# Kernel optimization log

Measured on AMD Instinct MI355X. Metric: run time of the kernel, lower is better.

The kernel has to match this reference:

```python
import jax, jax.numpy as jnp
import numpy as np

N_NODES = 50000


def sage_conv(x, src, dst, W_l, b_l, W_r, n_nodes):
    """PyG SAGEConv with mean aggregation: lin_l(mean_{j->i} x_j) + lin_r(x_i)."""
    msg = x[src]                                            # [E, d]
    agg = jax.ops.segment_sum(msg, dst, num_segments=n_nodes)
    cnt = jax.ops.segment_sum(jnp.ones((src.shape[0],), x.dtype), dst,
                              num_segments=n_nodes)
    agg = agg / jnp.maximum(cnt, 1.0)[:, None]              # mean over in-neighbors
    return agg @ W_l.T + b_l + x @ W_r.T


def setup_inputs() -> dict:
    key = jax.random.key(0)
    ks = jax.random.split(key, 8)
    d_in, d_hid, d_out = 128, 128, 64
    E = 600000
    x = jax.random.normal(ks[0], (N_NODES, d_in), dtype=jnp.float32)
    edge_index = jax.random.randint(ks[1], (2, E), 0, N_NODES, dtype=jnp.int64)
    s = 1.0 / np.sqrt(d_in)
    return {
        "x": x,
        "edge_index": edge_index,
        "W1_l": jax.random.normal(ks[2], (d_hid, d_in), jnp.float32) * s,
        "b1": jnp.zeros((d_hid,), jnp.float32),
        "W1_r": jax.random.normal(ks[3], (d_hid, d_in), jnp.float32) * s,
        "W2_l": jax.random.normal(ks[4], (d_out, d_hid), jnp.float32) * s,
        "b2": jnp.zeros((d_out,), jnp.float32),
        "W2_r": jax.random.normal(ks[5], (d_out, d_hid), jnp.float32) * s,
    }


def reference(x, edge_index, W1_l, b1, W1_r, W2_l, b2, W2_r):
    src, dst = edge_index[0], edge_index[1]
    h = sage_conv(x, src, dst, W1_l, b1, W1_r, N_NODES)
    h = jax.nn.relu(h)
    h = sage_conv(h, src, dst, W2_l, b2, W2_r, N_NODES)
    return jax.nn.log_softmax(h, axis=1)
```

## Files before the change

kernel.cpp:

```cpp
#include <hip/hip_runtime.h>
#include <math.h>

#define N_NODES 50000
#define D 128
#define D_OUT 64

typedef short bf16x8 __attribute__((ext_vector_type(8)));
typedef float f32x4  __attribute__((ext_vector_type(4)));
typedef unsigned short u16x8 __attribute__((ext_vector_type(8)));

__device__ __forceinline__ unsigned short f_to_bf16(float f) {
    unsigned int u = __float_as_uint(f);
    u = (u + 0x7fffu + ((u >> 16) & 1u)) >> 16;
    return (unsigned short)u;
}
__device__ __forceinline__ float bf16lo(unsigned int v) { return __uint_as_float(v << 16); }
__device__ __forceinline__ float bf16hi(unsigned int v) { return __uint_as_float(v & 0xffff0000u); }

__device__ __forceinline__ void conv8(const float* __restrict__ src, unsigned short* __restrict__ dst, int i)
{
    float4 v0 = *reinterpret_cast<const float4*>(src + i);
    float4 v1 = *reinterpret_cast<const float4*>(src + i + 4);
    u16x8 o;
    o[0] = f_to_bf16(v0.x); o[1] = f_to_bf16(v0.y);
    o[2] = f_to_bf16(v0.z); o[3] = f_to_bf16(v0.w);
    o[4] = f_to_bf16(v1.x); o[5] = f_to_bf16(v1.y);
    o[6] = f_to_bf16(v1.z); o[7] = f_to_bf16(v1.w);
    *reinterpret_cast<u16x8*>(dst + i) = o;
}

__device__ __forceinline__ void acc_add(float* acc, uint4 v)
{
    acc[0] += bf16lo(v.x); acc[1] += bf16hi(v.x);
    acc[2] += bf16lo(v.y); acc[3] += bf16hi(v.y);
    acc[4] += bf16lo(v.z); acc[5] += bf16hi(v.z);
    acc[6] += bf16lo(v.w); acc[7] += bf16hi(v.w);
}

__global__ __launch_bounds__(256) void zero_kernel(int* __restrict__ p, int n4)
{
    int i = blockIdx.x * 256 + threadIdx.x;
    if (i < n4) *reinterpret_cast<int4*>(p + i * 4) = make_int4(0, 0, 0, 0);
}

__global__ __launch_bounds__(256) void prep_kernel(
    const float* __restrict__ x, unsigned short* __restrict__ xb,
    const float* __restrict__ w1l, const float* __restrict__ w1r,
    const float* __restrict__ w2l, const float* __restrict__ w2r,
    unsigned short* __restrict__ Wb,
    const int* __restrict__ dst, int* __restrict__ deg,
    int XB, int E)
{
    const int bx = blockIdx.x;
    if (bx < XB) {
        int i = (bx * 256 + threadIdx.x) * 8;
        if (i < N_NODES * D) conv8(x, xb, i);
    } else if (bx < XB + 24) {
        int i = ((bx - XB) * 256 + threadIdx.x) * 8;
        const float* src; int off;
        if      (i < 16384) { src = w1l; off = 0; }
        else if (i < 32768) { src = w1r; off = 16384; }
        else if (i < 40960) { src = w2l; off = 32768; }
        else                { src = w2r; off = 40960; }
        conv8(src, Wb + off, i - off);
    } else {
        int e = (bx - XB - 24) * 256 + threadIdx.x;
        if (e < E) atomicAdd(&deg[dst[e]], 1);
    }
}

__global__ __launch_bounds__(256) void scan1_kernel(
    const int* __restrict__ deg, int* __restrict__ part,
    int* __restrict__ bsum, int n)
{
    const int t = threadIdx.x;
    const int base = blockIdx.x * 1024 + t * 4;

    int a0 = 0, a1 = 0, a2 = 0, a3 = 0;
    if (base + 3 < n) {
        int4 v = *reinterpret_cast<const int4*>(deg + base);
        a0 = v.x; a1 = v.y; a2 = v.z; a3 = v.w;
    } else if (base < n) {
        a0 = deg[base];
        if (base + 1 < n) a1 = deg[base + 1];
        if (base + 2 < n) a2 = deg[base + 2];
    }
    const int s0 = a0, s1 = s0 + a1, s2 = s1 + a2, s3 = s2 + a3;

    const int lane = t & 63;
    int incl = s3;
#pragma unroll
    for (int off = 1; off < 64; off <<= 1) {
        int up = __shfl_up(incl, off);
        if (lane >= off) incl += up;
    }

    __shared__ int wsum[4];
    const int wid = t >> 6;
    if (lane == 63) wsum[wid] = incl;
    __syncthreads();

    int woff = 0;
#pragma unroll
    for (int w = 0; w < 4; ++w) woff += (w < wid) ? wsum[w] : 0;

    const int ex = woff + incl - s3;
    if (base + 3 < n) {
        int4 o; o.x = ex; o.y = ex + s0; o.z = ex + s1; o.w = ex + s2;
        *reinterpret_cast<int4*>(part + base) = o;
    } else if (base < n) {
        part[base] = ex;
        if (base + 1 < n) part[base + 1] = ex + s0;
        if (base + 2 < n) part[base + 2] = ex + s1;
    }
    if (t == 255) bsum[blockIdx.x] = woff + incl;
}

__global__ __launch_bounds__(64) void scan2_kernel(
    int* __restrict__ bsum, int* __restrict__ row_ptr, int nb, int n)
{
    const int t = threadIdx.x;
    int v = (t < nb) ? bsum[t] : 0;
    int incl = v;
#pragma unroll
    for (int off = 1; off < 64; off <<= 1) {
        int up = __shfl_up(incl, off);
        if (t >= off) incl += up;
    }
    if (t < nb) bsum[t] = incl - v;
    if (t == 63) row_ptr[n] = incl;
}

__global__ __launch_bounds__(256) void scan3_kernel(
    const int* __restrict__ part, const int* __restrict__ bsum,
    int* __restrict__ row_ptr, int n)
{
    const int base = blockIdx.x * 1024 + threadIdx.x * 4;
    const int add = bsum[blockIdx.x];
    if (base + 3 < n) {
        int4 v = *reinterpret_cast<const int4*>(part + base);
        v.x += add; v.y += add; v.z += add; v.w += add;
        *reinterpret_cast<int4*>(row_ptr + base) = v;
    } else if (base < n) {
        row_ptr[base] = part[base] + add;
        if (base + 1 < n) row_ptr[base + 1] = part[base + 1] + add;
        if (base + 2 < n) row_ptr[base + 2] = part[base + 2] + add;
    }
}

__global__ __launch_bounds__(256) void fill_kernel(
    const int* __restrict__ src, const int* __restrict__ dst,
    const int* __restrict__ row_ptr, int* __restrict__ cursor,
    int* __restrict__ esrc, int E)
{
    int e = blockIdx.x * blockDim.x + threadIdx.x;
    if (e >= E) return;
    int d = dst[e];
    int pos = atomicAdd(&cursor[d], 1);
    esrc[row_ptr[d] + pos] = src[e];
}

__global__ __launch_bounds__(256) void gather_bf16_kernel(
    const unsigned short* __restrict__ xb,
    const int* __restrict__ row_ptr,
    const int* __restrict__ esrc,
    unsigned short* __restrict__ aggb,
    int n_nodes)
{
    const int wv   = threadIdx.x >> 6;
    const int lane = threadIdx.x & 63;
    const int node = blockIdx.x * 4 + wv;
    if (node >= n_nodes) return;

    const int beg = row_ptr[node];
    const int end = row_ptr[node + 1];
    const int g = lane >> 4;
    const int c = lane & 15;

    const uint4* x4 = reinterpret_cast<const uint4*>(xb);

    float acc[8];
#pragma unroll
    for (int k = 0; k < 8; ++k) acc[k] = 0.f;

    for (int base = beg; base < end; base += 64) {
        const int cnt = min(end - base, 64);
        int s = (base + lane < end) ? esrc[base + lane] : 0;
        for (int i = 0; i < cnt; i += 8) {
            const int p0 = i + g;
            const int p1 = i + 4 + g;
            const int s0 = __shfl(s, p0 & 63);
            const int s1 = __shfl(s, p1 & 63);
            uint4 v0 = x4[(size_t)s0 * 16 + c];
            uint4 v1 = x4[(size_t)s1 * 16 + c];
            if (p0 < cnt) acc_add(acc, v0);
            if (p1 < cnt) acc_add(acc, v1);
        }
    }

#pragma unroll
    for (int k = 0; k < 8; ++k) {
        acc[k] += __shfl_xor(acc[k], 16);
        acc[k] += __shfl_xor(acc[k], 32);
    }

    if (g == 0) {
        const float inv = (end > beg) ? 1.0f / (float)(end - beg) : 0.0f;
        uint4 o;
        o.x = (unsigned int)f_to_bf16(acc[0] * inv) | ((unsigned int)f_to_bf16(acc[1] * inv) << 16);
        o.y = (unsigned int)f_to_bf16(acc[2] * inv) | ((unsigned int)f_to_bf16(acc[3] * inv) << 16);
        o.z = (unsigned int)f_to_bf16(acc[4] * inv) | ((unsigned int)f_to_bf16(acc[5] * inv) << 16);
        o.w = (unsigned int)f_to_bf16(acc[6] * inv) | ((unsigned int)f_to_bf16(acc[7] * inv) << 16);
        reinterpret_cast<uint4*>(aggb)[(size_t)node * 16 + c] = o;
    }
}

__global__ __launch_bounds__(64) void layer1_mfma_kernel(
    const unsigned short* __restrict__ aggb,
    const unsigned short* __restrict__ xb,
    const unsigned short* __restrict__ Wb,
    const float* __restrict__ b1,
    unsigned short* __restrict__ h1b)
{
    const int lane  = threadIdx.x;
    const int node0 = blockIdx.x * 16;
    const int c16   = lane & 15;
    const int kg    = lane >> 4;

    bf16x8 a[2][4];
    {
        const unsigned short* A0 = aggb + (size_t)(node0 + c16) * D + kg * 8;
        const unsigned short* A1 = xb   + (size_t)(node0 + c16) * D + kg * 8;
#pragma unroll
        for (int kf = 0; kf < 4; ++kf) {
            a[0][kf] = *reinterpret_cast<const bf16x8*>(A0 + kf * 32);
            a[1][kf] = *reinterpret_cast<const bf16x8*>(A1 + kf * 32);
        }
    }
    const unsigned short* WL = Wb;
    const unsigned short* WR = Wb + 16384;

#pragma unroll 2
    for (int jt = 0; jt < 8; ++jt) {
        f32x4 acc = {0.f, 0.f, 0.f, 0.f};
        const unsigned short* wl = WL + (size_t)(jt * 16 + c16) * D + kg * 8;
        const unsigned short* wr = WR + (size_t)(jt * 16 + c16) * D + kg * 8;
#pragma unroll
        for (int kf = 0; kf < 4; ++kf) {
            bf16x8 b = *reinterpret_cast<const bf16x8*>(wl + kf * 32);
            acc = __builtin_amdgcn_mfma_f32_16x16x32_bf16(a[0][kf], b, acc, 0, 0, 0);
        }
#pragma unroll
        for (int kf = 0; kf < 4; ++kf) {
            bf16x8 b = *reinterpret_cast<const bf16x8*>(wr + kf * 32);
            acc = __builtin_amdgcn_mfma_f32_16x16x32_bf16(a[1][kf], b, acc, 0, 0, 0);
        }
        const float bias = b1[jt * 16 + c16];
#pragma unroll
        for (int i = 0; i < 4; ++i) {
            float v = fmaxf(acc[i] + bias, 0.0f);
            h1b[(size_t)(node0 + kg * 4 + i) * D + jt * 16 + c16] = f_to_bf16(v);
        }
    }
}

__global__ __launch_bounds__(64) void layer2_mfma_kernel(
    const unsigned short* __restrict__ aggb,
    const unsigned short* __restrict__ h1b,
    const unsigned short* __restrict__ Wb,
    const float* __restrict__ b2,
    float* __restrict__ out)
{
    const int lane  = threadIdx.x;
    const int node0 = blockIdx.x * 16;
    const int c16   = lane & 15;
    const int kg    = lane >> 4;

    bf16x8 a[2][4];
    {
        const unsigned short* A0 = aggb + (size_t)(node0 + c16) * D + kg * 8;
        const unsigned short* A1 = h1b  + (size_t)(node0 + c16) * D + kg * 8;
#pragma unroll
        for (int kf = 0; kf < 4; ++kf) {
            a[0][kf] = *reinterpret_cast<const bf16x8*>(A0 + kf * 32);
            a[1][kf] = *reinterpret_cast<const bf16x8*>(A1 + kf * 32);
        }
    }
    const unsigned short* WL = Wb + 32768;
    const unsigned short* WR = Wb + 40960;

    f32x4 accs[4];
#pragma unroll
    for (int jt = 0; jt < 4; ++jt) {
        f32x4 acc = {0.f, 0.f, 0.f, 0.f};
        const unsigned short* wl = WL + (size_t)(jt * 16 + c16) * D + kg * 8;
        const unsigned short* wr = WR + (size_t)(jt * 16 + c16) * D + kg * 8;
#pragma unroll
        for (int kf = 0; kf < 4; ++kf) {
            bf16x8 b = *reinterpret_cast<const bf16x8*>(wl + kf * 32);
            acc = __builtin_amdgcn_mfma_f32_16x16x32_bf16(a[0][kf], b, acc, 0, 0, 0);
        }
#pragma unroll
        for (int kf = 0; kf < 4; ++kf) {
            bf16x8 b = *reinterpret_cast<const bf16x8*>(wr + kf * 32);
            acc = __builtin_amdgcn_mfma_f32_16x16x32_bf16(a[1][kf], b, acc, 0, 0, 0);
        }
        accs[jt] = acc;
    }

    float bias[4];
#pragma unroll
    for (int jt = 0; jt < 4; ++jt) bias[jt] = b2[jt * 16 + c16];

#pragma unroll
    for (int i = 0; i < 4; ++i) {
        float z[4];
        float m = -1e30f;
#pragma unroll
        for (int jt = 0; jt < 4; ++jt) {
            z[jt] = accs[jt][i] + bias[jt];
            m = fmaxf(m, z[jt]);
        }
#pragma unroll
        for (int off = 1; off < 16; off <<= 1)
            m = fmaxf(m, __shfl_xor(m, off));
        float s = 0.f;
#pragma unroll
        for (int jt = 0; jt < 4; ++jt) s += expf(z[jt] - m);
#pragma unroll
        for (int off = 1; off < 16; off <<= 1)
            s += __shfl_xor(s, off);
        float lse = m + logf(s);
        const int node = node0 + kg * 4 + i;
#pragma unroll
        for (int jt = 0; jt < 4; ++jt)
            out[(size_t)node * D_OUT + jt * 16 + c16] = z[jt] - lse;
    }
}

extern "C" void kernel_launch(void* const* d_in, const int* in_sizes, int n_in,
                              void* d_out, int out_size, void* d_ws, size_t ws_size,
                              hipStream_t stream)
{
    const float* x   = (const float*)d_in[0];
    const int*   ei  = (const int*)d_in[1];
    const float* W1l = (const float*)d_in[2];
    const float* b1  = (const float*)d_in[3];
    const float* W1r = (const float*)d_in[4];
    const float* W2l = (const float*)d_in[5];
    const float* b2  = (const float*)d_in[6];
    const float* W2r = (const float*)d_in[7];
    float* out = (float*)d_out;

    const int E = in_sizes[1] / 2;
    const int* src = ei;
    const int* dst = ei + E;

    char* base = (char*)d_ws;
    size_t off = 0;
    auto take = [&](size_t bytes) { char* p = base + off; off += (bytes + 255) & ~(size_t)255; return p; };

    unsigned short* xb   = (unsigned short*)take((size_t)N_NODES * D * 2);
    unsigned short* aggb = (unsigned short*)take((size_t)N_NODES * D * 2);
    unsigned short* h1b  = (unsigned short*)take((size_t)N_NODES * D * 2);
    unsigned short* Wb   = (unsigned short*)take((size_t)49152 * 2);
    int* degcur  = (int*)take((size_t)2 * N_NODES * 4);
    int* deg     = degcur;
    int* cursor  = degcur + N_NODES;
    int* row_ptr = (int*)take(((size_t)N_NODES + 1) * 4);
    int* part    = (int*)take((size_t)N_NODES * 4);
    int* bsum    = (int*)take((size_t)64 * 4);
    int* esrc    = (int*)take((size_t)E * 4);

    const int EB = (E + 255) / 256;
    const int SB = (N_NODES + 1023) / 1024;
    const int XB = (N_NODES * D / 8 + 255) / 256;

    zero_kernel<<<(2 * N_NODES / 4 + 255) / 256, 256, 0, stream>>>(degcur, 2 * N_NODES / 4);
    prep_kernel<<<XB + 24 + EB, 256, 0, stream>>>(x, xb, W1l, W1r, W2l, W2r, Wb, dst, deg, XB, E);
    scan1_kernel<<<SB, 256, 0, stream>>>(deg, part, bsum, N_NODES);
    scan2_kernel<<<1, 64, 0, stream>>>(bsum, row_ptr, SB, N_NODES);
    scan3_kernel<<<SB, 256, 0, stream>>>(part, bsum, row_ptr, N_NODES);
    fill_kernel<<<EB, 256, 0, stream>>>(src, dst, row_ptr, cursor, esrc, E);

    const int GB = (N_NODES + 3) / 4;
    const int MB = N_NODES / 16;

    gather_bf16_kernel<<<GB, 256, 0, stream>>>(xb, row_ptr, esrc, aggb, N_NODES);
    layer1_mfma_kernel<<<MB, 64, 0, stream>>>(aggb, xb, Wb, b1, h1b);

    gather_bf16_kernel<<<GB, 256, 0, stream>>>(h1b, row_ptr, esrc, aggb, N_NODES);
    layer2_mfma_kernel<<<MB, 64, 0, stream>>>(aggb, h1b, Wb, b2, out);
}
```

Measured before the change: 173.5 us.

## Project layer-2 features before aggregation to halve second gather width

Mean aggregation is linear, so layer 2 now applies W2_l to h1 inside the layer-1 kernel (staged through shared memory) and writes a 64-wide bf16 projection. The second gather then averages 64-wide rows instead of 128-wide, halving the random gather traffic, and layer 2 adds the gathered result before the softmax. The gather kernel is templated on chunk count and issues more loads per iteration for memory-level parallelism. The cost is an extra projection write/read and an extra rounding to bf16 before aggregation.

After: 167.1 us. -3.7%, faster.

```diff
diff --git a/kernel.cpp b/kernel.cpp
--- a/kernel.cpp
+++ b/kernel.cpp
@@ -16,6 +16,7 @@
 }
 __device__ __forceinline__ float bf16lo(unsigned int v) { return __uint_as_float(v << 16); }
 __device__ __forceinline__ float bf16hi(unsigned int v) { return __uint_as_float(v & 0xffff0000u); }
+__device__ __forceinline__ float bf16f(unsigned short v) { return __uint_as_float((unsigned int)v << 16); }
 
 __device__ __forceinline__ void conv8(const float* __restrict__ src, unsigned short* __restrict__ dst, int i)
 {
@@ -160,6 +161,7 @@
     esrc[row_ptr[d] + pos] = src[e];
 }
 
+template<int CHUNKS>
 __global__ __launch_bounds__(256) void gather_bf16_kernel(
     const unsigned short* __restrict__ xb,
     const int* __restrict__ row_ptr,
@@ -167,6 +169,8 @@
     unsigned short* __restrict__ aggb,
     int n_nodes)
 {
+    constexpr int RPL = 64 / CHUNKS;
+    constexpr int NLOADS = 16 / RPL;
     const int wv   = threadIdx.x >> 6;
     const int lane = threadIdx.x & 63;
     const int node = blockIdx.x * 4 + wv;
@@ -174,8 +178,8 @@
 
     const int beg = row_ptr[node];
     const int end = row_ptr[node + 1];
-    const int g = lane >> 4;
-    const int c = lane & 15;
+    const int g = lane / CHUNKS;
+    const int c = lane % CHUNKS;
 
     const uint4* x4 = reinterpret_cast<const uint4*>(xb);
 
@@ -186,22 +190,26 @@
     for (int base = beg; base < end; base += 64) {
         const int cnt = min(end - base, 64);
         int s = (base + lane < end) ? esrc[base + lane] : 0;
-        for (int i = 0; i < cnt; i += 8) {
-            const int p0 = i + g;
-            const int p1 = i + 4 + g;
-            const int s0 = __shfl(s, p0 & 63);
-            const int s1 = __shfl(s, p1 & 63);
-            uint4 v0 = x4[(size_t)s0 * 16 + c];
-            uint4 v1 = x4[(size_t)s1 * 16 + c];
-            if (p0 < cnt) acc_add(acc, v0);
-            if (p1 < cnt) acc_add(acc, v1);
+        for (int i = 0; i < cnt; i += 16) {
+            int pp[NLOADS];
+            uint4 vv[NLOADS];
+#pragma unroll
+            for (int j = 0; j < NLOADS; ++j) {
+                pp[j] = i + j * RPL + g;
+                int sj = __shfl(s, pp[j]);
+                vv[j] = x4[(size_t)sj * CHUNKS + c];
+            }
+#pragma unroll
+            for (int j = 0; j < NLOADS; ++j)
+                if (pp[j] < cnt) acc_add(acc, vv[j]);
         }
     }
 
 #pragma unroll
     for (int k = 0; k < 8; ++k) {
-        acc[k] += __shfl_xor(acc[k], 16);
-        acc[k] += __shfl_xor(acc[k], 32);
+#pragma unroll
+        for (int off = CHUNKS; off < 64; off <<= 1)
+            acc[k] += __shfl_xor(acc[k], off);
     }
 
     if (g == 0) {
@@ -211,7 +219,7 @@
         o.y = (unsigned int)f_to_bf16(acc[2] * inv) | ((unsigned int)f_to_bf16(acc[3] * inv) << 16);
         o.z = (unsigned int)f_to_bf16(acc[4] * inv) | ((unsigned int)f_to_bf16(acc[5] * inv) << 16);
         o.w = (unsigned int)f_to_bf16(acc[6] * inv) | ((unsigned int)f_to_bf16(acc[7] * inv) << 16);
-        reinterpret_cast<uint4*>(aggb)[(size_t)node * 16 + c] = o;
+        reinterpret_cast<uint4*>(aggb)[(size_t)node * CHUNKS + c] = o;
     }
 }
 
@@ -220,8 +228,11 @@
     const unsigned short* __restrict__ xb,
     const unsigned short* __restrict__ Wb,
     const float* __restrict__ b1,
-    unsigned short* __restrict__ h1b)
-{
+    unsigned short* __restrict__ h1b,
+    unsigned short* __restrict__ t2b)
+{
+    __shared__ unsigned short h1s[16][144];
+
     const int lane  = threadIdx.x;
     const int node0 = blockIdx.x * 16;
     const int c16   = lane & 15;
@@ -259,13 +270,37 @@
 #pragma unroll
         for (int i = 0; i < 4; ++i) {
             float v = fmaxf(acc[i] + bias, 0.0f);
-            h1b[(size_t)(node0 + kg * 4 + i) * D + jt * 16 + c16] = f_to_bf16(v);
-        }
+            unsigned short us = f_to_bf16(v);
+            h1b[(size_t)(node0 + kg * 4 + i) * D + jt * 16 + c16] = us;
+            h1s[kg * 4 + i][jt * 16 + c16] = us;
+        }
+    }
+
+    __syncthreads();
+
+    bf16x8 a2[4];
+#pragma unroll
+    for (int kf = 0; kf < 4; ++kf)
+        a2[kf] = *reinterpret_cast<const bf16x8*>(&h1s[c16][kg * 8 + kf * 32]);
+
+    const unsigned short* W2L = Wb + 32768;
+#pragma unroll
+    for (int jt = 0; jt < 4; ++jt) {
+        f32x4 acc = {0.f, 0.f, 0.f, 0.f};
+        const unsigned short* wl = W2L + (size_t)(jt * 16 + c16) * D + kg * 8;
+#pragma unroll
+        for (int kf = 0; kf < 4; ++kf) {
+            bf16x8 b = *reinterpret_cast<const bf16x8*>(wl + kf * 32);
+            acc = __builtin_amdgcn_mfma_f32_16x16x32_bf16(a2[kf], b, acc, 0, 0, 0);
+        }
+#pragma unroll
+        for (int i = 0; i < 4; ++i)
+            t2b[(size_t)(node0 + kg * 4 + i) * D_OUT + jt * 16 + c16] = f_to_bf16(acc[i]);
     }
 }
 
 __global__ __launch_bounds__(64) void layer2_mfma_kernel(
-    const unsigned short* __restrict__ aggb,
+    const unsigned short* __restrict__ agg2b,
     const unsigned short* __restrict__ h1b,
     const unsigned short* __restrict__ Wb,
     const float* __restrict__ b2,
@@ -276,34 +311,24 @@
     const int c16   = lane & 15;
     const int kg    = lane >> 4;
 
-    bf16x8 a[2][4];
+    bf16x8 a[4];
     {
-        const unsigned short* A0 = aggb + (size_t)(node0 + c16) * D + kg * 8;
-        const unsigned short* A1 = h1b  + (size_t)(node0 + c16) * D + kg * 8;
-#pragma unroll
-        for (int kf = 0; kf < 4; ++kf) {
-            a[0][kf] = *reinterpret_cast<const bf16x8*>(A0 + kf * 32);
-            a[1][kf] = *reinterpret_cast<const bf16x8*>(A1 + kf * 32);
-        }
-    }
-    const unsigned short* WL = Wb + 32768;
+        const unsigned short* A1 = h1b + (size_t)(node0 + c16) * D + kg * 8;
+#pragma unroll
+        for (int kf = 0; kf < 4; ++kf)
+            a[kf] = *reinterpret_cast<const bf16x8*>(A1 + kf * 32);
+    }
     const unsigned short* WR = Wb + 40960;
 
     f32x4 accs[4];
 #pragma unroll
     for (int jt = 0; jt < 4; ++jt) {
         f32x4 acc = {0.f, 0.f, 0.f, 0.f};
-        const unsigned short* wl = WL + (size_t)(jt * 16 + c16) * D + kg * 8;
         const unsigned short* wr = WR + (size_t)(jt * 16 + c16) * D + kg * 8;
-#pragma unroll
-        for (int kf = 0; kf < 4; ++kf) {
-            bf16x8 b = *reinterpret_cast<const bf16x8*>(wl + kf * 32);
-            acc = __builtin_amdgcn_mfma_f32_16x16x32_bf16(a[0][kf], b, acc, 0, 0, 0);
-        }
 #pragma unroll
         for (int kf = 0; kf < 4; ++kf) {
             bf16x8 b = *reinterpret_cast<const bf16x8*>(wr + kf * 32);
-            acc = __builtin_amdgcn_mfma_f32_16x16x32_bf16(a[1][kf], b, acc, 0, 0, 0);
+            acc = __builtin_amdgcn_mfma_f32_16x16x32_bf16(a[kf], b, acc, 0, 0, 0);
         }
         accs[jt] = acc;
     }
@@ -314,11 +339,13 @@
 
 #pragma unroll
     for (int i = 0; i < 4; ++i) {
+        const int node = node0 + kg * 4 + i;
         float z[4];
         float m = -1e30f;
 #pragma unroll
         for (int jt = 0; jt < 4; ++jt) {
-            z[jt] = accs[jt][i] + bias[jt];
+            float lft = bf16f(agg2b[(size_t)node * D_OUT + jt * 16 + c16]);
+            z[jt] = lft + accs[jt][i] + bias[jt];
             m = fmaxf(m, z[jt]);
         }
 #pragma unroll
@@ -331,7 +358,6 @@
         for (int off = 1; off < 16; off <<= 1)
             s += __shfl_xor(s, off);
         float lse = m + logf(s);
-        const int node = node0 + kg * 4 + i;
 #pragma unroll
         for (int jt = 0; jt < 4; ++jt)
             out[(size_t)node * D_OUT + jt * 16 + c16] = z[jt] - lse;
@@ -360,10 +386,12 @@
     size_t off = 0;
     auto take = [&](size_t bytes) { char* p = base + off; off += (bytes + 255) & ~(size_t)255; return p; };
 
-    unsigned short* xb   = (unsigned short*)take((size_t)N_NODES * D * 2);
-    unsigned short* aggb = (unsigned short*)take((size_t)N_NODES * D * 2);
-    unsigned short* h1b  = (unsigned short*)take((size_t)N_NODES * D * 2);
-    unsigned short* Wb   = (unsigned short*)take((size_t)49152 * 2);
+    unsigned short* xb    = (unsigned short*)take((size_t)N_NODES * D * 2);
+    unsigned short* aggb  = (unsigned short*)take((size_t)N_NODES * D * 2);
+    unsigned short* h1b   = (unsigned short*)take((size_t)N_NODES * D * 2);
+    unsigned short* t2b   = (unsigned short*)take((size_t)N_NODES * D_OUT * 2);
+    unsigned short* agg2b = (unsigned short*)take((size_t)N_NODES * D_OUT * 2);
+    unsigned short* Wb    = (unsigned short*)take((size_t)49152 * 2);
     int* degcur  = (int*)take((size_t)2 * N_NODES * 4);
     int* deg     = degcur;
     int* cursor  = degcur + N_NODES;
@@ -386,9 +414,9 @@
     const int GB = (N_NODES + 3) / 4;
     const int MB = N_NODES / 16;
 
-    gather_bf16_kernel<<<GB, 256, 0, stream>>>(xb, row_ptr, esrc, aggb, N_NODES);
-    layer1_mfma_kernel<<<MB, 64, 0, stream>>>(aggb, xb, Wb, b1, h1b);
-
-    gather_bf16_kernel<<<GB, 256, 0, stream>>>(h1b, row_ptr, esrc, aggb, N_NODES);
-    layer2_mfma_kernel<<<MB, 64, 0, stream>>>(aggb, h1b, Wb, b2, out);
-}
+    gather_bf16_kernel<16><<<GB, 256, 0, stream>>>(xb, row_ptr, esrc, aggb, N_NODES);
+    layer1_mfma_kernel<<<MB, 64, 0, stream>>>(aggb, xb, Wb, b1, h1b, t2b);
+
+    gather_bf16_kernel<8><<<GB, 256, 0, stream>>>(t2b, row_ptr, esrc, agg2b, N_NODES);
+    layer2_mfma_kernel<<<MB, 64, 0, stream>>>(agg2b, h1b, Wb, b2, out);
+}
```
